# Performance work log

Hardware: AMD Instinct MI355X
Metric: run time of the kernel (lower is better)

## Reference

```python
import jax, jax.numpy as jnp
import numpy as np

EMBED_DIM = 1408
NUM_HEADS = 16
HEAD_DIM = EMBED_DIM // NUM_HEADS  # 88
SCALE = HEAD_DIM ** -0.5


def setup_inputs() -> dict:
    key = jax.random.key(0)
    k0, k1, k2, k3, k4 = jax.random.split(key, 5)
    B, S, D = 16, 577, EMBED_DIM
    hidden_states = jax.random.normal(k0, (B, S, D), dtype=jnp.float32)
    # fused QKV projection: [D, 3D] laid out as [q | k | v]
    w_qkv = jax.random.normal(k1, (D, 3 * D), dtype=jnp.float32) * (D ** -0.5)
    b_qkv = jax.random.normal(k2, (3 * D,), dtype=jnp.float32) * 0.02
    # output projection
    w_proj = jax.random.normal(k3, (D, D), dtype=jnp.float32) * (D ** -0.5)
    b_proj = jax.random.normal(k4, (D,), dtype=jnp.float32) * 0.02
    return {
        "hidden_states": hidden_states,
        "w_qkv": w_qkv,
        "b_qkv": b_qkv,
        "w_proj": w_proj,
        "b_proj": b_proj,
    }


def reference(hidden_states, w_qkv, b_qkv, w_proj, b_proj):
    B, S, D = hidden_states.shape
    H, Hd = NUM_HEADS, HEAD_DIM
    # fused QKV projection, then chunk along last dim (matches .chunk(3, -1))
    qkv = hidden_states @ w_qkv + b_qkv                      # [B, S, 3D]
    q, k, v = jnp.split(qkv, 3, axis=-1)                     # each [B, S, D]
    q = q.reshape(B, S, H, Hd)
    k = k.reshape(B, S, H, Hd)
    v = v.reshape(B, S, H, Hd)
    # scaled dot-product attention (no mask, no dropout at inference)
    scores = jnp.einsum("bqhd,bkhd->bhqk", q, k) * SCALE      # [B, H, S, S]
    probs = jax.nn.softmax(scores, axis=-1)
    out = jnp.einsum("bhqk,bkhd->bqhd", probs, v)             # [B, S, H, Hd]
    out = out.reshape(B, S, D)
    attn_output = out @ w_proj + b_proj                        # [B, S, D]
    return attn_output
```

## Files before the change

### kernel.cpp

```cpp
#include <hip/hip_runtime.h>
#include <cstddef>
#include <cstdint>

#define D_EMB   1408
#define NHEADS  16
#define HD      88
#define BATCH   16
#define SEQ     577
#define M_ROWS  (BATCH * SEQ)
#define N_QKV   (3 * D_EMB)
#define QKL_N   2816
#define SP      640
#define ATT_SCALE 0.10660035817780521f

#define QT 64
#define KT 64

typedef __attribute__((ext_vector_type(8))) short bf16x8;
typedef __attribute__((ext_vector_type(4))) float f32x4;
typedef unsigned short u16;

static __device__ __forceinline__ u16 f2bf(float x) {
  union { float f; unsigned u; } v; v.f = x;
  unsigned r = v.u + 0x7fff + ((v.u >> 16) & 1);
  return (u16)(r >> 16);
}
static __device__ __forceinline__ float bf2f(u16 h) {
  union { unsigned u; float f; } v; v.u = ((unsigned)h) << 16;
  return v.f;
}
static __device__ __forceinline__ void split_hl(float x, u16* hi, u16* lo) {
  u16 h = f2bf(x);
  *hi = h;
  *lo = f2bf(x - bf2f(h));
}

static __device__ __forceinline__ void async16(const u16* g, u16* l) {
  __builtin_amdgcn_global_load_lds(
      (const __attribute__((address_space(1))) unsigned int*)g,
      (__attribute__((address_space(3))) unsigned int*)l, 16, 0, 0);
}

__global__ __launch_bounds__(256)
void split_kernel(const float* __restrict__ X, u16* __restrict__ H,
                  u16* __restrict__ L, int n4) {
  int i = blockIdx.x * 256 + threadIdx.x;
  if (i >= n4) return;
  float4 v = ((const float4*)X)[i];
  ushort4 h, l;
  split_hl(v.x, &h.x, &l.x);
  split_hl(v.y, &h.y, &l.y);
  split_hl(v.z, &h.z, &l.z);
  split_hl(v.w, &h.w, &l.w);
  ((ushort4*)H)[i] = h;
  ((ushort4*)L)[i] = l;
}

__global__ __launch_bounds__(256)
void transpose_split_kernel(const float* __restrict__ W, u16* __restrict__ Th,
                            u16* __restrict__ Tl, int K, int N) {
  __shared__ float tile[32][33];
  const int n0 = blockIdx.x * 32, k0 = blockIdx.y * 32;
  const int tx = threadIdx.x & 31, ty = threadIdx.x >> 5;
#pragma unroll
  for (int i = 0; i < 4; ++i) {
    int k = ty + i * 8;
    tile[k][tx] = W[(size_t)(k0 + k) * N + n0 + tx];
  }
  __syncthreads();
#pragma unroll
  for (int i = 0; i < 4; ++i) {
    int n = ty + i * 8;
    float v = tile[tx][n];
    u16 h, l;
    split_hl(v, &h, &l);
    Th[(size_t)(n0 + n) * K + k0 + tx] = h;
    Tl[(size_t)(n0 + n) * K + k0 + tx] = l;
  }
}

__global__ __launch_bounds__(256)
void vtrans_kernel(const u16* __restrict__ qkvh, u16* __restrict__ vt) {
  __shared__ u16 tile[64][96];
  const int st = blockIdx.x, bh = blockIdx.y;
  const int b = bh >> 4, h = bh & 15;
  const int tid = threadIdx.x;
  const int s0 = st * 64;
  for (int idx = tid; idx < 64 * 22; idx += 256) {
    int j = idx / 22, c4 = (idx % 22) * 4;
    int s = s0 + j;
    ushort4 v = make_ushort4(0, 0, 0, 0);
    if (s < SEQ)
      v = *(const ushort4*)(qkvh + (size_t)(b * SEQ + s) * N_QKV + 2 * D_EMB + h * HD + c4);
    *(ushort4*)&tile[j][c4] = v;
  }
  if (tid < 64) {
    bf16x8 z = {0, 0, 0, 0, 0, 0, 0, 0};
    *(bf16x8*)&tile[tid][88] = z;
  }
  __syncthreads();
  for (int idx = tid; idx < 96 * 8; idx += 256) {
    int d = idx >> 3, c8 = (idx & 7) * 8;
    bf16x8 o;
#pragma unroll
    for (int e = 0; e < 8; ++e) o[e] = (short)tile[c8 + e][d];
    *(bf16x8*)(vt + ((size_t)bh * 96 + d) * SP + s0 + c8) = o;
  }
}

#define KDIM   1408
#define BMT    256
#define BNT    128
#define SLOT_E 24576
#define AS_H   0
#define AS_L   8192
#define BS_H   16384
#define BS_L   20480

#define STAGE_A0(SLOTP, SSN)                                              \
  {                                                                       \
    const int k0s = (SSN) * 32;                                           \
    u16* Ls = &Lds[SLOTP][0];                                             \
    async16(Ah + srcA0 + k0s, Ls + AS_H + ldsA0);                         \
    async16(Al + srcA0 + k0s, Ls + AS_L + ldsA0);                         \
  }
#define STAGE_A1(SLOTP, SSN)                                              \
  {                                                                       \
    const int k0s = (SSN) * 32;                                           \
    u16* Ls = &Lds[SLOTP][0];                                             \
    async16(Ah + srcA1 + k0s, Ls + AS_H + ldsA1);                         \
    async16(Al + srcA1 + k0s, Ls + AS_L + ldsA1);                         \
  }
#define STAGE_B(SLOTP, SSN)                                               \
  {                                                                       \
    const int k0s = (SSN) * 32;                                           \
    u16* Ls = &Lds[SLOTP][0];                                             \
    async16(Bh + srcB0 + k0s, Ls + BS_H + ldsB0);                         \
    async16(Bl + srcB0 + k0s, Ls + BS_L + ldsB0);                         \
  }

#define MFMA3(I, J)                                                                               \
  acc[I][J] = __builtin_amdgcn_mfma_f32_16x16x32_bf16(fah[I], fbh[J], acc[I][J], 0, 0, 0);        \
  acc[I][J] = __builtin_amdgcn_mfma_f32_16x16x32_bf16(fah[I], fbl[J], acc[I][J], 0, 0, 0);        \
  acc[I][J] = __builtin_amdgcn_mfma_f32_16x16x32_bf16(fal[I], fbh[J], acc[I][J], 0, 0, 0);

#define PH_SYNC                                                           \
  __builtin_amdgcn_s_barrier();                                           \
  asm volatile("s_waitcnt lgkmcnt(0)" ::: "memory");                      \
  __builtin_amdgcn_sched_barrier(0);

#define SLOT_RUN(PHYS, NXPHYS, SSN, DO_STAGE, VM)                         \
  {                                                                       \
    const u16* Lb = &Lds[PHYS][0];                                        \
    bf16x8 fah[4], fal[4], fbh[4], fbl[4];                                \
                                 \
    fah[0] = *(const bf16x8*)&Lb[AS_H + offA[0]];                         \
    fah[1] = *(const bf16x8*)&Lb[AS_H + offA[1]];                         \
    fal[0] = *(const bf16x8*)&Lb[AS_L + offA[0]];                         \
    fal[1] = *(const bf16x8*)&Lb[AS_L + offA[1]];                         \
    fbh[0] = *(const bf16x8*)&Lb[BS_H + offB[0]];                         \
    fbh[1] = *(const bf16x8*)&Lb[BS_H + offB[1]];                         \
    fbl[0] = *(const bf16x8*)&Lb[BS_L + offB[0]];                         \
    fbl[1] = *(const bf16x8*)&Lb[BS_L + offB[1]];                         \
    if (DO_STAGE) STAGE_A0(NXPHYS, SSN);                                  \
    PH_SYNC                                                               \
    __builtin_amdgcn_s_setprio(1);                                        \
    MFMA3(0, 0) MFMA3(0, 1) MFMA3(1, 0) MFMA3(1, 1)                       \
    __builtin_amdgcn_s_setprio(0);                                        \
    __builtin_amdgcn_s_barrier();                                         \
                                 \
    fbh[2] = *(const bf16x8*)&Lb[BS_H + offB[2]];                         \
    fbh[3] = *(const bf16x8*)&Lb[BS_H + offB[3]];                         \
    fbl[2] = *(const bf16x8*)&Lb[BS_L + offB[2]];                         \
    fbl[3] = *(const bf16x8*)&Lb[BS_L + offB[3]];                         \
    if (DO_STAGE) STAGE_A1(NXPHYS, SSN);                                  \
    PH_SYNC                                                               \
    __builtin_amdgcn_s_setprio(1);                                        \
    MFMA3(0, 2) MFMA3(0, 3) MFMA3(1, 2) MFMA3(1, 3)                       \
    __builtin_amdgcn_s_setprio(0);                                        \
    __builtin_amdgcn_s_barrier();                                         \
                               \
    fah[2] = *(const bf16x8*)&Lb[AS_H + offA[2]];                         \
    fah[3] = *(const bf16x8*)&Lb[AS_H + offA[3]];                         \
    fal[2] = *(const bf16x8*)&Lb[AS_L + offA[2]];                         \
    fal[3] = *(const bf16x8*)&Lb[AS_L + offA[3]];                         \
    if (DO_STAGE) STAGE_B(NXPHYS, SSN);                                   \
    PH_SYNC                                                               \
    __builtin_amdgcn_s_setprio(1);                                        \
    MFMA3(2, 2) MFMA3(2, 3) MFMA3(3, 2) MFMA3(3, 3)                       \
    MFMA3(2, 0) MFMA3(2, 1) MFMA3(3, 0) MFMA3(3, 1)                       \
    __builtin_amdgcn_s_setprio(0);                                        \
    asm volatile("s_waitcnt vmcnt(" #VM ")" ::: "memory");                \
    __builtin_amdgcn_s_barrier();                                         \
  }

template <int MODE>
__global__ __launch_bounds__(512)
void gemm8p_kernel(const u16* __restrict__ Ah, const u16* __restrict__ Al,
                   const u16* __restrict__ Bh, const u16* __restrict__ Bl,
                   const float* __restrict__ bias,
                   float* __restrict__ Cf, u16* __restrict__ Ch, u16* __restrict__ Cl,
                   int M, int N, int NX) {
  const int lin  = blockIdx.x;
  const int xcd  = lin & 7;
  const int t    = lin >> 3;
  const int band = xcd + 8 * (t / NX);
  const int bm0  = band * BMT;
  if (bm0 >= M) return;
  const int bn0  = (t % NX) * BNT;

  __shared__ u16 Lds[3][SLOT_E];

  const int tid  = threadIdx.x;
  const int lane = tid & 63;
  const int w    = tid >> 6;
  const int quad = lane >> 4, lc = lane & 15;
  const int wm   = w >> 1, wn = w & 1;

  size_t srcA0, srcA1, srcB0;
  int ldsA0, ldsA1, ldsB0;
  {
    int r0 = tid >> 2, q0 = tid & 3;
    int ra0 = bm0 + r0; if (ra0 > M - 1) ra0 = M - 1;
    srcA0 = (size_t)ra0 * KDIM + (size_t)((q0 ^ ((r0 >> 1) & 3)) * 8);
    ldsA0 = w * 512;
    int r1 = 128 + r0;
    int ra1 = bm0 + r1; if (ra1 > M - 1) ra1 = M - 1;
    srcA1 = (size_t)ra1 * KDIM + (size_t)((q0 ^ ((r1 >> 1) & 3)) * 8);
    ldsA1 = 4096 + w * 512;
    srcB0 = (size_t)(bn0 + r0) * KDIM + (size_t)((q0 ^ ((r0 >> 1) & 3)) * 8);
    ldsB0 = w * 512;
  }

  int offA[4], offB[4];
  {
    const int qphys = quad ^ ((lc >> 1) & 3);
#pragma unroll
    for (int i = 0; i < 4; ++i) {
      offA[i] = (wm * 64 + i * 16 + lc) * 32 + qphys * 8;
      offB[i] = (wn * 64 + i * 16 + lc) * 32 + qphys * 8;
    }
  }

  f32x4 acc[4][4];
#pragma unroll
  for (int i = 0; i < 4; ++i)
#pragma unroll
    for (int j = 0; j < 4; ++j) acc[i][j] = (f32x4){0.f, 0.f, 0.f, 0.f};

  STAGE_A0(0, 0); STAGE_A1(0, 0); STAGE_B(0, 0);
  STAGE_A0(1, 1); STAGE_A1(1, 1); STAGE_B(1, 1);
  asm volatile("s_waitcnt vmcnt(6)" ::: "memory");
  __builtin_amdgcn_s_barrier();

#pragma unroll 1
  for (int u = 0; u < 14; ++u) {
    const int s = u * 3;
    SLOT_RUN(0, 2, s + 2, true, 6);
    SLOT_RUN(1, 0, s + 3, true, 6);
    SLOT_RUN(2, 1, s + 4, true, 6);
  }
  SLOT_RUN(0, 0, 0, false, 0);
  SLOT_RUN(1, 0, 0, false, 0);

#pragma unroll
  for (int j = 0; j < 4; ++j) {
    int col = bn0 + wn * 64 + j * 16 + lc;
    float bj = bias[col];
#pragma unroll
    for (int i = 0; i < 4; ++i) {
#pragma unroll
      for (int rg = 0; rg < 4; ++rg) {
        int row = bm0 + wm * 64 + i * 16 + quad * 4 + rg;
        if (row < M) {
          float v = acc[i][j][rg] + bj;
          if (MODE == 0) {
            Cf[(size_t)row * N + col] = v;
          } else {
            u16 hh, ll;
            split_hl(v, &hh, &ll);
            Ch[(size_t)row * N + col] = hh;
            if (col < QKL_N) Cl[(size_t)row * QKL_N + col] = ll;
          }
        }
      }
    }
  }
}

__global__ __launch_bounds__(256)
void attn_kernel2(const u16* __restrict__ qkvh, const u16* __restrict__ qkvl,
                  const u16* __restrict__ vt,
                  u16* __restrict__ outh, u16* __restrict__ outl) {
  __shared__ u16 Khi[KT][104];
  __shared__ u16 Klo[KT][104];
  __shared__ u16 Vs[96][72];
  __shared__ u16 Pb[QT][72];

  const int tid  = threadIdx.x;
  const int lane = tid & 63;
  const int wv   = tid >> 6;
  const int quad = lane >> 4;
  const int lc   = lane & 15;

  const int qt = blockIdx.x, h = blockIdx.y, b = blockIdx.z;
  const int q0 = qt * QT;

  if (tid < KT) {
    bf16x8 z = {0, 0, 0, 0, 0, 0, 0, 0};
    *(bf16x8*)&Khi[tid][88] = z;
    *(bf16x8*)&Klo[tid][88] = z;
  }

  bf16x8 qh[3], ql[3];
  {
    const bf16x8 z = {0, 0, 0, 0, 0, 0, 0, 0};
    int qrow = q0 + wv * 16 + lc;
    bool qv = qrow < SEQ;
    size_t bh_ = (size_t)(b * SEQ + (qv ? qrow : 0));
#pragma unroll
    for (int ks = 0; ks < 3; ++ks) {
      if (!qv || (ks == 2 && quad == 3)) {
        qh[ks] = z; ql[ks] = z;
      } else {
        qh[ks] = *(const bf16x8*)(qkvh + bh_ * N_QKV + h * HD + ks * 32 + quad * 8);
        ql[ks] = *(const bf16x8*)(qkvl + bh_ * QKL_N + h * HD + ks * 32 + quad * 8);
      }
    }
  }

  float mrow[4], lrow[4];
#pragma unroll
  for (int r = 0; r < 4; ++r) { mrow[r] = -INFINITY; lrow[r] = 0.f; }
  f32x4 oacc[6];
#pragma unroll
  for (int nn = 0; nn < 6; ++nn) oacc[nn] = (f32x4){0.f, 0.f, 0.f, 0.f};

  const u16* vsrc = vt + (size_t)(b * 16 + h) * 96 * SP;

  for (int kt = 0; kt < SP / KT; ++kt) {
    const int k0 = kt * KT;
    __syncthreads();

    for (int idx = tid; idx < KT * 22; idx += 256) {
      int j = idx / 22, c4 = (idx % 22) * 4;
      int s = k0 + j;
      ushort4 kh = make_ushort4(0, 0, 0, 0), kl = make_ushort4(0, 0, 0, 0);
      if (s < SEQ) {
        size_t rb = (size_t)(b * SEQ + s);
        kh = *(const ushort4*)(qkvh + rb * N_QKV + D_EMB + h * HD + c4);
        kl = *(const ushort4*)(qkvl + rb * QKL_N + D_EMB + h * HD + c4);
      }
      *(ushort4*)&Khi[j][c4] = kh;
      *(ushort4*)&Klo[j][c4] = kl;
    }
    for (int idx = tid; idx < 96 * 8; idx += 256) {
      int d = idx >> 3, c8 = (idx & 7) * 8;
      *(bf16x8*)&Vs[d][c8] = *(const bf16x8*)(vsrc + (size_t)d * SP + k0 + c8);
    }
    __syncthreads();

    f32x4 sc[4];
#pragma unroll
    for (int t = 0; t < 4; ++t) {
      f32x4 a = (f32x4){0.f, 0.f, 0.f, 0.f};
#pragma unroll
      for (int ks = 0; ks < 3; ++ks) {
        bf16x8 kh = *(const bf16x8*)&Khi[t * 16 + lc][ks * 32 + quad * 8];
        bf16x8 kl = *(const bf16x8*)&Klo[t * 16 + lc][ks * 32 + quad * 8];
        a = __builtin_amdgcn_mfma_f32_16x16x32_bf16(qh[ks], kh, a, 0, 0, 0);
        a = __builtin_amdgcn_mfma_f32_16x16x32_bf16(qh[ks], kl, a, 0, 0, 0);
        a = __builtin_amdgcn_mfma_f32_16x16x32_bf16(ql[ks], kh, a, 0, 0, 0);
      }
      sc[t] = a;
    }
#pragma unroll
    for (int t = 0; t < 4; ++t) {
      bool valid = (k0 + t * 16 + lc) < SEQ;
#pragma unroll
      for (int r = 0; r < 4; ++r)
        sc[t][r] = valid ? sc[t][r] * ATT_SCALE : -INFINITY;
    }

    float alpha[4];
#pragma unroll
    for (int r = 0; r < 4; ++r) {
      float v = fmaxf(fmaxf(sc[0][r], sc[1][r]), fmaxf(sc[2][r], sc[3][r]));
      v = fmaxf(v, __shfl_xor(v, 1));
      v = fmaxf(v, __shfl_xor(v, 2));
      v = fmaxf(v, __shfl_xor(v, 4));
      v = fmaxf(v, __shfl_xor(v, 8));
      float mnew = fmaxf(mrow[r], v);
      alpha[r] = expf(mrow[r] - mnew);
      mrow[r] = mnew;
      float s = 0.f;
#pragma unroll
      for (int t = 0; t < 4; ++t) {
        float p = expf(sc[t][r] - mnew);
        sc[t][r] = p;
        s += p;
      }
      s += __shfl_xor(s, 1);
      s += __shfl_xor(s, 2);
      s += __shfl_xor(s, 4);
      s += __shfl_xor(s, 8);
      lrow[r] = lrow[r] * alpha[r] + s;
    }
#pragma unroll
    for (int t = 0; t < 4; ++t)
#pragma unroll
      for (int r = 0; r < 4; ++r)
        Pb[wv * 16 + quad * 4 + r][t * 16 + lc] = f2bf(sc[t][r]);
#pragma unroll
    for (int nn = 0; nn < 6; ++nn)
#pragma unroll
      for (int r = 0; r < 4; ++r) oacc[nn][r] *= alpha[r];
    __syncthreads();

    bf16x8 p0 = *(const bf16x8*)&Pb[wv * 16 + lc][quad * 8];
    bf16x8 p1 = *(const bf16x8*)&Pb[wv * 16 + lc][32 + quad * 8];
#pragma unroll
    for (int nn = 0; nn < 6; ++nn) {
      bf16x8 v0 = *(const bf16x8*)&Vs[nn * 16 + lc][quad * 8];
      bf16x8 v1 = *(const bf16x8*)&Vs[nn * 16 + lc][32 + quad * 8];
      oacc[nn] = __builtin_amdgcn_mfma_f32_16x16x32_bf16(p0, v0, oacc[nn], 0, 0, 0);
      oacc[nn] = __builtin_amdgcn_mfma_f32_16x16x32_bf16(p1, v1, oacc[nn], 0, 0, 0);
    }
  }

#pragma unroll
  for (int r = 0; r < 4; ++r) {
    int s = q0 + wv * 16 + quad * 4 + r;
    if (s < SEQ) {
      float inv = 1.f / lrow[r];
      size_t base = (size_t)(b * SEQ + s) * D_EMB + h * HD;
#pragma unroll
      for (int nn = 0; nn < 6; ++nn) {
        int d = nn * 16 + lc;
        if (d < HD) {
          float v = oacc[nn][r] * inv;
          u16 hh, ll;
          split_hl(v, &hh, &ll);
          outh[base + d] = hh;
          outl[base + d] = ll;
        }
      }
    }
  }
}

extern "C" void kernel_launch(void* const* d_in, const int* in_sizes, int n_in,
                              void* d_out, int out_size, void* d_ws, size_t ws_size,
                              hipStream_t stream) {
  const float* hs    = (const float*)d_in[0];
  const float* wqkv  = (const float*)d_in[1];
  const float* bqkv  = (const float*)d_in[2];
  const float* wproj = (const float*)d_in[3];
  const float* bproj = (const float*)d_in[4];
  float* out = (float*)d_out;

  u16* qkvH = (u16*)d_ws;
  u16* qkvL = qkvH + (size_t)M_ROWS * N_QKV;
  u16* hsH  = qkvL + (size_t)M_ROWS * QKL_N;
  u16* hsL  = hsH + (size_t)M_ROWS * D_EMB;
  u16* vt   = hsL + (size_t)M_ROWS * D_EMB;
  u16* wtH  = vt;
  u16* wtL  = wtH + (size_t)N_QKV * D_EMB;
  u16* attnH = hsH;
  u16* attnL = hsL;

  {
    int n4 = (M_ROWS * D_EMB) / 4;
    split_kernel<<<(n4 + 255) / 256, 256, 0, stream>>>(hs, hsH, hsL, n4);
  }
  {
    dim3 g(N_QKV / 32, D_EMB / 32);
    transpose_split_kernel<<<g, 256, 0, stream>>>(wqkv, wtH, wtL, D_EMB, N_QKV);
  }
  {
    gemm8p_kernel<1><<<33 * 40, 512, 0, stream>>>(hsH, hsL, wtH, wtL, bqkv,
                                                  nullptr, qkvH, qkvL,
                                                  M_ROWS, N_QKV, 33);
  }
  {
    dim3 g(SP / 64, BATCH * NHEADS);
    vtrans_kernel<<<g, 256, 0, stream>>>(qkvH, vt);
  }
  {
    dim3 g(SP / QT, NHEADS, BATCH);
    attn_kernel2<<<g, 256, 0, stream>>>(qkvH, qkvL, vt, attnH, attnL);
  }
  {
    dim3 g(D_EMB / 32, D_EMB / 32);
    transpose_split_kernel<<<g, 256, 0, stream>>>(wproj, wtH, wtL, D_EMB, D_EMB);
  }
  {
    gemm8p_kernel<0><<<11 * 40, 512, 0, stream>>>(attnH, attnL, wtH, wtL, bproj,
                                                  out, nullptr, nullptr,
                                                  M_ROWS, D_EMB, 11);
  }
}
```

Baseline: 888.6 us.

## Enlarge GEMM tile to 256x256 with double-buffered LDS pipeline

Widens the split-bf16 GEMM block tile from 256x128 to 256x256, with each of the 8 waves computing a 128x64 sub-tile (8x4 accumulators). The LDS ring drops from three slots to two, with a full vmcnt(0) wait each slot, and N-edge clamping and guards are added so the tile can overhang N. The aim is better operand reuse per LDS load and fewer global loads per FLOP. In exchange it doubles accumulator registers, shrinks the grid (wasting compute on the N overhang for 4224 and 1408), and gives less prefetch depth to hide latency.

After: 867.0 us. 2.4% less time.

```diff
diff --git a/kernel.cpp b/kernel.cpp
--- a/kernel.cpp
+++ b/kernel.cpp
@@ -110,87 +110,103 @@
 
 #define KDIM   1408
 #define BMT    256
-#define BNT    128
-#define SLOT_E 24576
+#define BNT    256
+#define SLOT_E 32768
 #define AS_H   0
 #define AS_L   8192
 #define BS_H   16384
-#define BS_L   20480
-
-#define STAGE_A0(SLOTP, SSN)                                              \
+#define BS_L   24576
+
+#define STG_A(SLOTP, SSN)                                                 \
   {                                                                       \
     const int k0s = (SSN) * 32;                                           \
     u16* Ls = &Lds[SLOTP][0];                                             \
-    async16(Ah + srcA0 + k0s, Ls + AS_H + ldsA0);                         \
-    async16(Al + srcA0 + k0s, Ls + AS_L + ldsA0);                         \
-  }
-#define STAGE_A1(SLOTP, SSN)                                              \
+    async16(Ah + srcA0 + k0s, Ls + AS_H + ldsD0);                         \
+    async16(Al + srcA0 + k0s, Ls + AS_L + ldsD0);                         \
+    async16(Ah + srcA1 + k0s, Ls + AS_H + ldsD1);                         \
+    async16(Al + srcA1 + k0s, Ls + AS_L + ldsD1);                         \
+  }
+#define STG_B(SLOTP, SSN)                                                 \
   {                                                                       \
     const int k0s = (SSN) * 32;                                           \
     u16* Ls = &Lds[SLOTP][0];                                             \
-    async16(Ah + srcA1 + k0s, Ls + AS_H + ldsA1);                         \
-    async16(Al + srcA1 + k0s, Ls + AS_L + ldsA1);                         \
-  }
-#define STAGE_B(SLOTP, SSN)                                               \
-  {                                                                       \
-    const int k0s = (SSN) * 32;                                           \
-    u16* Ls = &Lds[SLOTP][0];                                             \
-    async16(Bh + srcB0 + k0s, Ls + BS_H + ldsB0);                         \
-    async16(Bl + srcB0 + k0s, Ls + BS_L + ldsB0);                         \
-  }
-
-#define MFMA3(I, J)                                                                               \
-  acc[I][J] = __builtin_amdgcn_mfma_f32_16x16x32_bf16(fah[I], fbh[J], acc[I][J], 0, 0, 0);        \
-  acc[I][J] = __builtin_amdgcn_mfma_f32_16x16x32_bf16(fah[I], fbl[J], acc[I][J], 0, 0, 0);        \
-  acc[I][J] = __builtin_amdgcn_mfma_f32_16x16x32_bf16(fal[I], fbh[J], acc[I][J], 0, 0, 0);
+    async16(Bh + srcB0 + k0s, Ls + BS_H + ldsD0);                         \
+    async16(Bl + srcB0 + k0s, Ls + BS_L + ldsD0);                         \
+    async16(Bh + srcB1 + k0s, Ls + BS_H + ldsD1);                         \
+    async16(Bl + srcB1 + k0s, Ls + BS_L + ldsD1);                         \
+  }
+
+#define MFMA3(ACC, AH, AL, BH, BL)                                                  \
+  ACC = __builtin_amdgcn_mfma_f32_16x16x32_bf16(AH, BH, ACC, 0, 0, 0);              \
+  ACC = __builtin_amdgcn_mfma_f32_16x16x32_bf16(AH, BL, ACC, 0, 0, 0);              \
+  ACC = __builtin_amdgcn_mfma_f32_16x16x32_bf16(AL, BH, ACC, 0, 0, 0);
+
+#define ROW_MFMA(I, AH, AL)                                               \
+  MFMA3(acc[I][0], AH, AL, fbh0, fbl0)                                    \
+  MFMA3(acc[I][1], AH, AL, fbh1, fbl1)                                    \
+  MFMA3(acc[I][2], AH, AL, fbh2, fbl2)                                    \
+  MFMA3(acc[I][3], AH, AL, fbh3, fbl3)
 
 #define PH_SYNC                                                           \
   __builtin_amdgcn_s_barrier();                                           \
   asm volatile("s_waitcnt lgkmcnt(0)" ::: "memory");                      \
   __builtin_amdgcn_sched_barrier(0);
 
-#define SLOT_RUN(PHYS, NXPHYS, SSN, DO_STAGE, VM)                         \
+#define SLOT_RUN(PHYS, SSN, DO_STAGE, DO_VM)                              \
   {                                                                       \
     const u16* Lb = &Lds[PHYS][0];                                        \
-    bf16x8 fah[4], fal[4], fbh[4], fbl[4];                                \
-                                 \
-    fah[0] = *(const bf16x8*)&Lb[AS_H + offA[0]];                         \
-    fah[1] = *(const bf16x8*)&Lb[AS_H + offA[1]];                         \
-    fal[0] = *(const bf16x8*)&Lb[AS_L + offA[0]];                         \
-    fal[1] = *(const bf16x8*)&Lb[AS_L + offA[1]];                         \
-    fbh[0] = *(const bf16x8*)&Lb[BS_H + offB[0]];                         \
-    fbh[1] = *(const bf16x8*)&Lb[BS_H + offB[1]];                         \
-    fbl[0] = *(const bf16x8*)&Lb[BS_L + offB[0]];                         \
-    fbl[1] = *(const bf16x8*)&Lb[BS_L + offB[1]];                         \
-    if (DO_STAGE) STAGE_A0(NXPHYS, SSN);                                  \
+    bf16x8 fbh0, fbh1, fbh2, fbh3, fbl0, fbl1, fbl2, fbl3;                \
+    bf16x8 a0h, a0l, a1h, a1l;                                            \
+                              \
+    fbh0 = *(const bf16x8*)&Lb[BS_H + offB[0]];                           \
+    fbh1 = *(const bf16x8*)&Lb[BS_H + offB[1]];                           \
+    fbh2 = *(const bf16x8*)&Lb[BS_H + offB[2]];                           \
+    fbh3 = *(const bf16x8*)&Lb[BS_H + offB[3]];                           \
+    fbl0 = *(const bf16x8*)&Lb[BS_L + offB[0]];                           \
+    fbl1 = *(const bf16x8*)&Lb[BS_L + offB[1]];                           \
+    fbl2 = *(const bf16x8*)&Lb[BS_L + offB[2]];                           \
+    fbl3 = *(const bf16x8*)&Lb[BS_L + offB[3]];                           \
+    a0h = *(const bf16x8*)&Lb[AS_H + offA[0]];                            \
+    a0l = *(const bf16x8*)&Lb[AS_L + offA[0]];                            \
+    a1h = *(const bf16x8*)&Lb[AS_H + offA[1]];                            \
+    a1l = *(const bf16x8*)&Lb[AS_L + offA[1]];                            \
+    if (DO_STAGE) STG_A(PHYS ^ 1, SSN);                                   \
     PH_SYNC                                                               \
     __builtin_amdgcn_s_setprio(1);                                        \
-    MFMA3(0, 0) MFMA3(0, 1) MFMA3(1, 0) MFMA3(1, 1)                       \
+    ROW_MFMA(0, a0h, a0l) ROW_MFMA(1, a1h, a1l)                           \
     __builtin_amdgcn_s_setprio(0);                                        \
     __builtin_amdgcn_s_barrier();                                         \
-                                 \
-    fbh[2] = *(const bf16x8*)&Lb[BS_H + offB[2]];                         \
-    fbh[3] = *(const bf16x8*)&Lb[BS_H + offB[3]];                         \
-    fbl[2] = *(const bf16x8*)&Lb[BS_L + offB[2]];                         \
-    fbl[3] = *(const bf16x8*)&Lb[BS_L + offB[3]];                         \
-    if (DO_STAGE) STAGE_A1(NXPHYS, SSN);                                  \
+                                           \
+    a0h = *(const bf16x8*)&Lb[AS_H + offA[2]];                            \
+    a0l = *(const bf16x8*)&Lb[AS_L + offA[2]];                            \
+    a1h = *(const bf16x8*)&Lb[AS_H + offA[3]];                            \
+    a1l = *(const bf16x8*)&Lb[AS_L + offA[3]];                            \
+    if (DO_STAGE) STG_B(PHYS ^ 1, SSN);                                   \
     PH_SYNC                                                               \
     __builtin_amdgcn_s_setprio(1);                                        \
-    MFMA3(0, 2) MFMA3(0, 3) MFMA3(1, 2) MFMA3(1, 3)                       \
+    ROW_MFMA(2, a0h, a0l) ROW_MFMA(3, a1h, a1l)                           \
     __builtin_amdgcn_s_setprio(0);                                        \
     __builtin_amdgcn_s_barrier();                                         \
-                               \
-    fah[2] = *(const bf16x8*)&Lb[AS_H + offA[2]];                         \
-    fah[3] = *(const bf16x8*)&Lb[AS_H + offA[3]];                         \
-    fal[2] = *(const bf16x8*)&Lb[AS_L + offA[2]];                         \
-    fal[3] = *(const bf16x8*)&Lb[AS_L + offA[3]];                         \
-    if (DO_STAGE) STAGE_B(NXPHYS, SSN);                                   \
+                                           \
+    a0h = *(const bf16x8*)&Lb[AS_H + offA[4]];                            \
+    a0l = *(const bf16x8*)&Lb[AS_L + offA[4]];                            \
+    a1h = *(const bf16x8*)&Lb[AS_H + offA[5]];                            \
+    a1l = *(const bf16x8*)&Lb[AS_L + offA[5]];                            \
     PH_SYNC                                                               \
     __builtin_amdgcn_s_setprio(1);                                        \
-    MFMA3(2, 2) MFMA3(2, 3) MFMA3(3, 2) MFMA3(3, 3)                       \
-    MFMA3(2, 0) MFMA3(2, 1) MFMA3(3, 0) MFMA3(3, 1)                       \
+    ROW_MFMA(4, a0h, a0l) ROW_MFMA(5, a1h, a1l)                           \
     __builtin_amdgcn_s_setprio(0);                                        \
-    asm volatile("s_waitcnt vmcnt(" #VM ")" ::: "memory");                \
+    __builtin_amdgcn_s_barrier();                                         \
+                                           \
+    a0h = *(const bf16x8*)&Lb[AS_H + offA[6]];                            \
+    a0l = *(const bf16x8*)&Lb[AS_L + offA[6]];                            \
+    a1h = *(const bf16x8*)&Lb[AS_H + offA[7]];                            \
+    a1l = *(const bf16x8*)&Lb[AS_L + offA[7]];                            \
+    PH_SYNC                                                               \
+    __builtin_amdgcn_s_setprio(1);                                        \
+    ROW_MFMA(6, a0h, a0l) ROW_MFMA(7, a1h, a1l)                           \
+    __builtin_amdgcn_s_setprio(0);                                        \
+    if (DO_VM) asm volatile("s_waitcnt vmcnt(0)" ::: "memory");           \
     __builtin_amdgcn_s_barrier();                                         \
   }
 
@@ -209,78 +225,83 @@
   if (bm0 >= M) return;
   const int bn0  = (t % NX) * BNT;
 
-  __shared__ u16 Lds[3][SLOT_E];
+  __shared__ u16 Lds[2][SLOT_E];
 
   const int tid  = threadIdx.x;
   const int lane = tid & 63;
   const int w    = tid >> 6;
   const int quad = lane >> 4, lc = lane & 15;
-  const int wm   = w >> 1, wn = w & 1;
-
-  size_t srcA0, srcA1, srcB0;
-  int ldsA0, ldsA1, ldsB0;
+  const int wm   = w >> 2, wn = w & 3;
+
+  size_t srcA0, srcA1, srcB0, srcB1;
+  int ldsD0, ldsD1;
   {
     int r0 = tid >> 2, q0 = tid & 3;
+    int swz0 = (q0 ^ ((r0 >> 1) & 3)) * 8;
+    int r1 = 128 + r0;
+    int swz1 = (q0 ^ ((r1 >> 1) & 3)) * 8;
     int ra0 = bm0 + r0; if (ra0 > M - 1) ra0 = M - 1;
-    srcA0 = (size_t)ra0 * KDIM + (size_t)((q0 ^ ((r0 >> 1) & 3)) * 8);
-    ldsA0 = w * 512;
-    int r1 = 128 + r0;
     int ra1 = bm0 + r1; if (ra1 > M - 1) ra1 = M - 1;
-    srcA1 = (size_t)ra1 * KDIM + (size_t)((q0 ^ ((r1 >> 1) & 3)) * 8);
-    ldsA1 = 4096 + w * 512;
-    srcB0 = (size_t)(bn0 + r0) * KDIM + (size_t)((q0 ^ ((r0 >> 1) & 3)) * 8);
-    ldsB0 = w * 512;
-  }
-
-  int offA[4], offB[4];
+    srcA0 = (size_t)ra0 * KDIM + swz0;
+    srcA1 = (size_t)ra1 * KDIM + swz1;
+    int rb0 = bn0 + r0; if (rb0 > N - 1) rb0 = N - 1;
+    int rb1 = bn0 + r1; if (rb1 > N - 1) rb1 = N - 1;
+    srcB0 = (size_t)rb0 * KDIM + swz0;
+    srcB1 = (size_t)rb1 * KDIM + swz1;
+    ldsD0 = w * 512;
+    ldsD1 = 4096 + w * 512;
+  }
+
+  int offA[8], offB[4];
   {
     const int qphys = quad ^ ((lc >> 1) & 3);
 #pragma unroll
-    for (int i = 0; i < 4; ++i) {
-      offA[i] = (wm * 64 + i * 16 + lc) * 32 + qphys * 8;
-      offB[i] = (wn * 64 + i * 16 + lc) * 32 + qphys * 8;
-    }
-  }
-
-  f32x4 acc[4][4];
-#pragma unroll
-  for (int i = 0; i < 4; ++i)
+    for (int i = 0; i < 8; ++i)
+      offA[i] = (wm * 128 + i * 16 + lc) * 32 + qphys * 8;
+#pragma unroll
+    for (int j = 0; j < 4; ++j)
+      offB[j] = (wn * 64 + j * 16 + lc) * 32 + qphys * 8;
+  }
+
+  f32x4 acc[8][4];
+#pragma unroll
+  for (int i = 0; i < 8; ++i)
 #pragma unroll
     for (int j = 0; j < 4; ++j) acc[i][j] = (f32x4){0.f, 0.f, 0.f, 0.f};
 
-  STAGE_A0(0, 0); STAGE_A1(0, 0); STAGE_B(0, 0);
-  STAGE_A0(1, 1); STAGE_A1(1, 1); STAGE_B(1, 1);
-  asm volatile("s_waitcnt vmcnt(6)" ::: "memory");
+  STG_A(0, 0);
+  STG_B(0, 0);
+  asm volatile("s_waitcnt vmcnt(0)" ::: "memory");
   __builtin_amdgcn_s_barrier();
 
 #pragma unroll 1
-  for (int u = 0; u < 14; ++u) {
-    const int s = u * 3;
-    SLOT_RUN(0, 2, s + 2, true, 6);
-    SLOT_RUN(1, 0, s + 3, true, 6);
-    SLOT_RUN(2, 1, s + 4, true, 6);
-  }
-  SLOT_RUN(0, 0, 0, false, 0);
-  SLOT_RUN(1, 0, 0, false, 0);
+  for (int u = 0; u < 21; ++u) {
+    SLOT_RUN(0, 2 * u + 1, true, true);
+    SLOT_RUN(1, 2 * u + 2, true, true);
+  }
+  SLOT_RUN(0, 43, true, true);
+  SLOT_RUN(1, 0, false, false);
 
 #pragma unroll
   for (int j = 0; j < 4; ++j) {
     int col = bn0 + wn * 64 + j * 16 + lc;
-    float bj = bias[col];
-#pragma unroll
-    for (int i = 0; i < 4; ++i) {
-#pragma unroll
-      for (int rg = 0; rg < 4; ++rg) {
-        int row = bm0 + wm * 64 + i * 16 + quad * 4 + rg;
-        if (row < M) {
-          float v = acc[i][j][rg] + bj;
-          if (MODE == 0) {
-            Cf[(size_t)row * N + col] = v;
-          } else {
-            u16 hh, ll;
-            split_hl(v, &hh, &ll);
-            Ch[(size_t)row * N + col] = hh;
-            if (col < QKL_N) Cl[(size_t)row * QKL_N + col] = ll;
+    if (col < N) {
+      float bj = bias[col];
+#pragma unroll
+      for (int i = 0; i < 8; ++i) {
+#pragma unroll
+        for (int rg = 0; rg < 4; ++rg) {
+          int row = bm0 + wm * 128 + i * 16 + quad * 4 + rg;
+          if (row < M) {
+            float v = acc[i][j][rg] + bj;
+            if (MODE == 0) {
+              Cf[(size_t)row * N + col] = v;
+            } else {
+              u16 hh, ll;
+              split_hl(v, &hh, &ll);
+              Ch[(size_t)row * N + col] = hh;
+              if (col < QKL_N) Cl[(size_t)row * QKL_N + col] = ll;
+            }
           }
         }
       }
@@ -478,9 +499,9 @@
     transpose_split_kernel<<<g, 256, 0, stream>>>(wqkv, wtH, wtL, D_EMB, N_QKV);
   }
   {
-    gemm8p_kernel<1><<<33 * 40, 512, 0, stream>>>(hsH, hsL, wtH, wtL, bqkv,
+    gemm8p_kernel<1><<<17 * 40, 512, 0, stream>>>(hsH, hsL, wtH, wtL, bqkv,
                                                   nullptr, qkvH, qkvL,
-                                                  M_ROWS, N_QKV, 33);
+                                                  M_ROWS, N_QKV, 17);
   }
   {
     dim3 g(SP / 64, BATCH * NHEADS);
@@ -495,8 +516,8 @@
     transpose_split_kernel<<<g, 256, 0, stream>>>(wproj, wtH, wtL, D_EMB, D_EMB);
   }
   {
-    gemm8p_kernel<0><<<11 * 40, 512, 0, stream>>>(attnH, attnL, wtH, wtL, bproj,
-                                                  out, nullptr, nullptr,
-                                                  M_ROWS, D_EMB, 11);
-  }
-}
+    gemm8p_kernel<0><<<6 * 40, 512, 0, stream>>>(attnH, attnL, wtH, wtL, bproj,
+                                                 out, nullptr, nullptr,
+                                                 M_ROWS, D_EMB, 6);
+  }
+}
```
